# Kernel tuning notes

Hardware: AMD Instinct MI355X
Metric: run time of the kernel (lower is better)

## Reference

```python
import jax, jax.numpy as jnp
import numpy as np

N_NODES = 100000


def gcn_conv(x, W, b, row, col, ew, n_nodes):
    """PyG GCNConv: add self-loops (weight 1), symmetric normalization,
    out[c] = sum_{(r,c) in E} norm * (x @ W)[r] + b."""
    sl = jnp.arange(n_nodes, dtype=row.dtype)
    row2 = jnp.concatenate([row, sl])
    col2 = jnp.concatenate([col, sl])
    ew2 = jnp.concatenate([ew, jnp.ones((n_nodes,), dtype=ew.dtype)])
    deg = jax.ops.segment_sum(ew2, col2, num_segments=n_nodes)  # [N]
    dinv = jnp.where(deg > 0, jax.lax.rsqrt(jnp.where(deg > 0, deg, 1.0)), 0.0)
    norm = dinv[row2] * ew2 * dinv[col2]                         # [E+N]
    h = x @ W                                                    # [N, out]
    msg = h[row2] * norm[:, None]                                # gather + scale
    out = jax.ops.segment_sum(msg, col2, num_segments=n_nodes)   # scatter-add
    return out + b


def setup_inputs() -> dict:
    key = jax.random.key(0)
    k1, k2, k3, k4, k5 = jax.random.split(key, 5)
    F_IN, HID, C = 512, 16, 40
    E = 3200000
    x = jax.random.normal(k1, (N_NODES, F_IN), dtype=jnp.float32)
    edge_index = jax.random.randint(k2, (2, E), 0, N_NODES, dtype=jnp.int64)
    edge_weight = jax.random.uniform(k3, (E,), dtype=jnp.float32)
    # Glorot-ish init for weights
    W1 = jax.random.normal(k4, (F_IN, HID), dtype=jnp.float32) / np.sqrt(F_IN)
    b1 = jnp.zeros((HID,), dtype=jnp.float32)
    W2 = jax.random.normal(k5, (HID, C), dtype=jnp.float32) / np.sqrt(HID)
    b2 = jnp.zeros((C,), dtype=jnp.float32)
    return {"x": x, "edge_index": edge_index, "edge_weight": edge_weight,
            "W1": W1, "b1": b1, "W2": W2, "b2": b2}


def reference(x, edge_index, edge_weight, W1, b1, W2, b2):
    row, col = edge_index[0], edge_index[1]
    h = jax.nn.relu(gcn_conv(x, W1, b1, row, col, edge_weight, N_NODES))
    # dropout p=0.1 is identity at inference; DFALayer/DFA are identity in forward
    logits = gcn_conv(h, W2, b2, row, col, edge_weight, N_NODES)
    return jax.nn.log_softmax(logits, axis=1)
```

## Files before the change

### kernel.cpp

```cpp
#include <hip/hip_runtime.h>
#include <hip/hip_bf16.h>
#include <math.h>

#define F_IN 512
#define HID  16
#define C_OUT 40

#define BSH    7
#define BNODES 128
#define MAXNB  1024

#define EPB 8192
#define CTH 512

__device__ __forceinline__ unsigned short f2bf(float f) {
    unsigned u = __float_as_uint(f);
    unsigned r = (u + 0x7FFF + ((u >> 16) & 1)) >> 16;
    return (unsigned short)r;
}
__device__ __forceinline__ float bf2f(unsigned short h) {
    return __uint_as_float(((unsigned)h) << 16);
}

__global__ __launch_bounds__(1024) void k_zero(int* __restrict__ g, int n) {
    int t = threadIdx.x;
    if (t < n) g[t] = 0;
}

__global__ __launch_bounds__(CTH) void k_count(const int* __restrict__ col,
                                               int* __restrict__ gcnt,
                                               int E, int NB) {
    __shared__ int lc[MAXNB];
    int t = threadIdx.x;
    for (int i = t; i < NB; i += CTH) lc[i] = 0;
    __syncthreads();
    int base = blockIdx.x * EPB;
#pragma unroll
    for (int i = 0; i < EPB / CTH; ++i) {
        int e = base + t + i * CTH;
        if (e < E) atomicAdd(&lc[col[e] >> BSH], 1);
    }
    __syncthreads();
    for (int i = t; i < NB; i += CTH)
        if (lc[i]) atomicAdd(&gcnt[i], lc[i]);
}

__global__ __launch_bounds__(1024) void k_scan(const int* __restrict__ gcnt,
                                               int* __restrict__ bo,
                                               int* __restrict__ bcur,
                                               int* __restrict__ offs,
                                               int NB, int N, int E) {
    __shared__ int s[1024];
    int t = threadIdx.x;
    int v = (t < NB) ? gcnt[t] : 0;
    s[t] = v;
    __syncthreads();
    for (int off = 1; off < 1024; off <<= 1) {
        int x = (t >= off) ? s[t - off] : 0;
        __syncthreads();
        s[t] += x;
        __syncthreads();
    }
    if (t < NB) { int o = s[t] - v; bo[t] = o; bcur[t] = o; }
    if (t == 0) { bo[NB] = E; offs[N] = E; }
}

__global__ __launch_bounds__(CTH) void k_part(const int* __restrict__ row,
                                              const int* __restrict__ col,
                                              const float* __restrict__ ew,
                                              int* __restrict__ bcur,
                                              int2* __restrict__ st,
                                              int E, int NB) {
    __shared__ int lc[MAXNB];
    __shared__ int lb[MAXNB];
    int t = threadIdx.x;
    for (int i = t; i < NB; i += CTH) lc[i] = 0;
    __syncthreads();
    int base = blockIdx.x * EPB;
#pragma unroll
    for (int i = 0; i < EPB / CTH; ++i) {
        int e = base + t + i * CTH;
        if (e < E) atomicAdd(&lc[col[e] >> BSH], 1);
    }
    __syncthreads();
    for (int i = t; i < NB; i += CTH) {
        int c = lc[i];
        lb[i] = c ? atomicAdd(&bcur[i], c) : 0;
    }
    __syncthreads();
    for (int i = t; i < NB; i += CTH) lc[i] = 0;
    __syncthreads();
#pragma unroll
    for (int i = 0; i < EPB / CTH; ++i) {
        int e = base + t + i * CTH;
        if (e < E) {
            int c = col[e];
            int b = c >> BSH;
            int r = atomicAdd(&lc[b], 1);
            st[lb[b] + r] = make_int2((row[e] << BSH) | (c & (BNODES - 1)),
                                      __float_as_int(ew[e]));
        }
    }
}

__global__ __launch_bounds__(256) void k_sort(const int* __restrict__ bo,
                                              const int2* __restrict__ st,
                                              int2* __restrict__ st2,
                                              int* __restrict__ offs,
                                              float* __restrict__ dinv, int N) {
    __shared__ int cnt[BNODES];
    __shared__ float wsum[BNODES];
    __shared__ int off[BNODES];
    int t = threadIdx.x;
    int b = blockIdx.x;
    if (t < BNODES) { cnt[t] = 0; wsum[t] = 0.0f; }
    __syncthreads();
    int beg = bo[b], end = bo[b + 1];
    for (int e = beg + t; e < end; e += 256) {
        int2 rec = st[e];
        int cl = rec.x & (BNODES - 1);
        atomicAdd(&cnt[cl], 1);
        atomicAdd(&wsum[cl], __int_as_float(rec.y));
    }
    __syncthreads();
    if (t < BNODES) off[t] = cnt[t];
    __syncthreads();
    for (int o = 1; o < BNODES; o <<= 1) {
        int v = (t < BNODES && t >= o) ? off[t - o] : 0;
        __syncthreads();
        if (t < BNODES) off[t] += v;
        __syncthreads();
    }
    if (t < BNODES) {
        int ex = off[t] - cnt[t];
        off[t] = ex;
        int n = b * BNODES + t;
        if (n < N) {
            offs[n] = beg + ex;
            dinv[n] = rsqrtf(1.0f + wsum[t]);
        }
        cnt[t] = 0;
    }
    __syncthreads();
    for (int e = beg + t; e < end; e += 256) {
        int2 rec = st[e];
        int cl = rec.x & (BNODES - 1);
        int r = atomicAdd(&cnt[cl], 1);
        st2[beg + off[cl] + r] = make_int2(rec.x >> BSH, rec.y);
    }
}

__global__ __launch_bounds__(256) void k_gemm1(const float* __restrict__ x,
                                               const float* __restrict__ W,
                                               const float* __restrict__ dinv,
                                               unsigned short* __restrict__ hb,
                                               int N) {
    int n = blockIdx.x * 256 + threadIdx.x;
    if (n >= N) return;
    float acc[HID];
#pragma unroll
    for (int j = 0; j < HID; ++j) acc[j] = 0.0f;
    const float4* xr = (const float4*)(x + (size_t)n * F_IN);
#pragma unroll 4
    for (int k4 = 0; k4 < F_IN / 4; ++k4) {
        float4 xv = xr[k4];
        const float* wk = W + k4 * 4 * HID;
#pragma unroll
        for (int j = 0; j < HID; ++j) acc[j] += xv.x * wk[j];
#pragma unroll
        for (int j = 0; j < HID; ++j) acc[j] += xv.y * wk[HID + j];
#pragma unroll
        for (int j = 0; j < HID; ++j) acc[j] += xv.z * wk[2 * HID + j];
#pragma unroll
        for (int j = 0; j < HID; ++j) acc[j] += xv.w * wk[3 * HID + j];
    }
    float d = dinv[n];
    unsigned pk[8];
#pragma unroll
    for (int j = 0; j < 8; ++j)
        pk[j] = (unsigned)f2bf(d * acc[2 * j]) |
                ((unsigned)f2bf(d * acc[2 * j + 1]) << 16);
    uint4* hp = (uint4*)(hb + (size_t)n * HID);
    hp[0] = make_uint4(pk[0], pk[1], pk[2], pk[3]);
    hp[1] = make_uint4(pk[4], pk[5], pk[6], pk[7]);
}

__global__ __launch_bounds__(256) void k_agg1(const int* __restrict__ offs,
                                              const int2* __restrict__ st2,
                                              const float* __restrict__ dinv,
                                              const unsigned short* __restrict__ srcb,
                                              const float* __restrict__ bias,
                                              unsigned short* __restrict__ dstb,
                                              int N) {
    int t = threadIdx.x;
    int lane = t & 63, w = t >> 6;
    int n = blockIdx.x * 4 + w;
    if (n >= N) return;
    int q = lane & 3, i = lane >> 2;
    int beg = offs[n], end = offs[n + 1];
    float4 acc = make_float4(0.f, 0.f, 0.f, 0.f);
    for (int e = beg + i; e < end; e += 16) {
        int2 rec = st2[e];
        float wt = __int_as_float(rec.y);
        ushort4 v = ((const ushort4*)(srcb + (size_t)rec.x * HID))[q];
        acc.x += wt * bf2f(v.x);
        acc.y += wt * bf2f(v.y);
        acc.z += wt * bf2f(v.z);
        acc.w += wt * bf2f(v.w);
    }
#pragma unroll
    for (int off = 4; off < 64; off <<= 1) {
        acc.x += __shfl_xor(acc.x, off, 64);
        acc.y += __shfl_xor(acc.y, off, 64);
        acc.z += __shfl_xor(acc.z, off, 64);
        acc.w += __shfl_xor(acc.w, off, 64);
    }
    if (i == 0) {
        float d = dinv[n];
        ushort4 sv = ((const ushort4*)(srcb + (size_t)n * HID))[q];
        float4 bq = ((const float4*)bias)[q];
        float r0 = d * fmaxf(d * (acc.x + bf2f(sv.x)) + bq.x, 0.f);
        float r1 = d * fmaxf(d * (acc.y + bf2f(sv.y)) + bq.y, 0.f);
        float r2 = d * fmaxf(d * (acc.z + bf2f(sv.z)) + bq.z, 0.f);
        float r3 = d * fmaxf(d * (acc.w + bf2f(sv.w)) + bq.w, 0.f);
        ((ushort4*)(dstb + (size_t)n * HID))[q] =
            make_ushort4(f2bf(r0), f2bf(r1), f2bf(r2), f2bf(r3));
    }
}

__global__ __launch_bounds__(256) void k_agg2(const int* __restrict__ offs,
                                              const int2* __restrict__ st2,
                                              const float* __restrict__ dinv,
                                              const unsigned short* __restrict__ srcb,
                                              const float* __restrict__ W2,
                                              const float* __restrict__ b2,
                                              float* __restrict__ out, int N) {
    __shared__ float Ws[HID * C_OUT];
    __shared__ float bs[C_OUT];
    int t = threadIdx.x;
    for (int iw = t; iw < HID * C_OUT; iw += 256) Ws[iw] = W2[iw];
    if (t < C_OUT) bs[t] = b2[t];
    __syncthreads();

    int lane = t & 63, w = t >> 6;
    int n = blockIdx.x * 4 + w;
    if (n >= N) return;
    int q = lane & 3, i = lane >> 2;
    int beg = offs[n], end = offs[n + 1];
    float4 acc = make_float4(0.f, 0.f, 0.f, 0.f);
    for (int e = beg + i; e < end; e += 16) {
        int2 rec = st2[e];
        float wt = __int_as_float(rec.y);
        ushort4 v = ((const ushort4*)(srcb + (size_t)rec.x * HID))[q];
        acc.x += wt * bf2f(v.x);
        acc.y += wt * bf2f(v.y);
        acc.z += wt * bf2f(v.z);
        acc.w += wt * bf2f(v.w);
    }
#pragma unroll
    for (int off = 4; off < 64; off <<= 1) {
        acc.x += __shfl_xor(acc.x, off, 64);
        acc.y += __shfl_xor(acc.y, off, 64);
        acc.z += __shfl_xor(acc.z, off, 64);
        acc.w += __shfl_xor(acc.w, off, 64);
    }
    float d = dinv[n];
    ushort4 sv = ((const ushort4*)(srcb + (size_t)n * HID))[q];
    float gq[4];
    gq[0] = d * (acc.x + bf2f(sv.x));
    gq[1] = d * (acc.y + bf2f(sv.y));
    gq[2] = d * (acc.z + bf2f(sv.z));
    gq[3] = d * (acc.w + bf2f(sv.w));
    float g16[16];
    int base = lane & ~3;
#pragma unroll
    for (int qq = 0; qq < 4; ++qq) {
#pragma unroll
        for (int k = 0; k < 4; ++k)
            g16[qq * 4 + k] = __shfl(gq[k], base + qq, 64);
    }
    float logit = -INFINITY;
    if (lane < C_OUT) {
        float a = bs[lane];
#pragma unroll
        for (int j = 0; j < HID; ++j) a += g16[j] * Ws[j * C_OUT + lane];
        logit = a;
    }
    float m = logit;
#pragma unroll
    for (int off = 32; off > 0; off >>= 1) m = fmaxf(m, __shfl_xor(m, off, 64));
    float ex = (lane < C_OUT) ? __expf(logit - m) : 0.0f;
    float s = ex;
#pragma unroll
    for (int off = 32; off > 0; off >>= 1) s += __shfl_xor(s, off, 64);
    if (lane < C_OUT) out[(size_t)n * C_OUT + lane] = logit - m - __logf(s);
}

extern "C" void kernel_launch(void* const* d_in, const int* in_sizes, int n_in,
                              void* d_out, int out_size, void* d_ws, size_t ws_size,
                              hipStream_t stream) {
    const float* x   = (const float*)d_in[0];
    const int*   ei  = (const int*)d_in[1];
    const float* ew  = (const float*)d_in[2];
    const float* W1  = (const float*)d_in[3];
    const float* b1  = (const float*)d_in[4];
    const float* W2  = (const float*)d_in[5];
    const float* b2  = (const float*)d_in[6];
    float* out = (float*)d_out;

    const int N = in_sizes[0] / F_IN;
    const int E = in_sizes[2];
    const int* row = ei;
    const int* col = ei + E;
    const int NB = (N + BNODES - 1) >> BSH;

    int* wsi = (int*)d_ws;
    size_t o = 0;
    int* gcnt  = wsi + o; o += MAXNB;
    int* bo    = wsi + o; o += MAXNB + 1;
    int* bcur  = wsi + o; o += MAXNB;
    int* offs  = wsi + o; o += (size_t)N + 8;
    float* dinv = (float*)(wsi + o); o += N;
    unsigned short* h1b = (unsigned short*)(wsi + o); o += (size_t)N * HID / 2;
    unsigned short* a1b = (unsigned short*)(wsi + o); o += (size_t)N * HID / 2;
    int2* st   = (int2*)(wsi + o); o += (size_t)E * 2;
    int2* st2  = (int2*)(wsi + o); o += (size_t)E * 2;

    int gC = (E + EPB - 1) / EPB;
    int gW = (N + 3) / 4;

    k_zero<<<1, 1024, 0, stream>>>(gcnt, NB);
    k_count<<<gC, CTH, 0, stream>>>(col, gcnt, E, NB);
    k_scan<<<1, 1024, 0, stream>>>(gcnt, bo, bcur, offs, NB, N, E);
    k_part<<<gC, CTH, 0, stream>>>(row, col, ew, bcur, st, E, NB);
    k_sort<<<NB, 256, 0, stream>>>(bo, st, st2, offs, dinv, N);
    k_gemm1<<<(N + 255) / 256, 256, 0, stream>>>(x, W1, dinv, h1b, N);
    k_agg1<<<gW, 256, 0, stream>>>(offs, st2, dinv, h1b, b1, a1b, N);
    k_agg2<<<gW, 256, 0, stream>>>(offs, st2, dinv, a1b, W2, b2, out, N);
}
```

Measured before the change: 631.5 us.

## Pack CSR edges to 32 bits, precompute partition offsets, split GEMM K across waves

Three changes land together. Sorted edge records shrink from int2 to one 32-bit word: a 17-bit source index and a 15-bit bf16 edge weight with the sign bit dropped. This halves the edge traffic in both aggregation passes, at the cost of weight precision. k_count now writes per-block histograms and a new k_scan2 turns them into per-block offsets, so k_part no longer recounts edges or does global atomics. k_gemm1 splits the K dimension across four waves per 64-node tile and reduces them with LDS atomics, which raises parallelism and memory-level parallelism for the x read.

Measured after the change: 667.6 us. +5.7%, slower.

```diff
diff --git a/kernel.cpp b/kernel.cpp
--- a/kernel.cpp
+++ b/kernel.cpp
@@ -21,6 +21,9 @@
 __device__ __forceinline__ float bf2f(unsigned short h) {
     return __uint_as_float(((unsigned)h) << 16);
 }
+__device__ __forceinline__ unsigned ew15(unsigned u) {
+    return ((u + 0x7FFF + ((u >> 16) & 1)) >> 16) & 0x7FFF;
+}
 
 __global__ __launch_bounds__(1024) void k_zero(int* __restrict__ g, int n) {
     int t = threadIdx.x;
@@ -28,6 +31,7 @@
 }
 
 __global__ __launch_bounds__(CTH) void k_count(const int* __restrict__ col,
+                                               int* __restrict__ bh,
                                                int* __restrict__ gcnt,
                                                int E, int NB) {
     __shared__ int lc[MAXNB];
@@ -41,13 +45,16 @@
         if (e < E) atomicAdd(&lc[col[e] >> BSH], 1);
     }
     __syncthreads();
-    for (int i = t; i < NB; i += CTH)
-        if (lc[i]) atomicAdd(&gcnt[i], lc[i]);
+    int* bhrow = bh + (size_t)blockIdx.x * MAXNB;
+    for (int i = t; i < NB; i += CTH) {
+        int c = lc[i];
+        bhrow[i] = c;
+        if (c) atomicAdd(&gcnt[i], c);
+    }
 }
 
 __global__ __launch_bounds__(1024) void k_scan(const int* __restrict__ gcnt,
                                                int* __restrict__ bo,
-                                               int* __restrict__ bcur,
                                                int* __restrict__ offs,
                                                int NB, int N, int E) {
     __shared__ int s[1024];
@@ -61,35 +68,36 @@
         s[t] += x;
         __syncthreads();
     }
-    if (t < NB) { int o = s[t] - v; bo[t] = o; bcur[t] = o; }
+    if (t < NB) bo[t] = s[t] - v;
     if (t == 0) { bo[NB] = E; offs[N] = E; }
+}
+
+__global__ __launch_bounds__(128) void k_scan2(const int* __restrict__ bo,
+                                               const int* __restrict__ bh,
+                                               int* __restrict__ bb,
+                                               int NB, int NBLK) {
+    int t = blockIdx.x * 128 + threadIdx.x;
+    if (t >= NB) return;
+    int base = bo[t];
+    for (int blk = 0; blk < NBLK; ++blk) {
+        bb[(size_t)blk * MAXNB + t] = base;
+        base += bh[(size_t)blk * MAXNB + t];
+    }
 }
 
 __global__ __launch_bounds__(CTH) void k_part(const int* __restrict__ row,
                                               const int* __restrict__ col,
                                               const float* __restrict__ ew,
-                                              int* __restrict__ bcur,
+                                              const int* __restrict__ bb,
                                               int2* __restrict__ st,
                                               int E, int NB) {
     __shared__ int lc[MAXNB];
     __shared__ int lb[MAXNB];
     int t = threadIdx.x;
-    for (int i = t; i < NB; i += CTH) lc[i] = 0;
+    const int* bbrow = bb + (size_t)blockIdx.x * MAXNB;
+    for (int i = t; i < NB; i += CTH) { lc[i] = 0; lb[i] = bbrow[i]; }
     __syncthreads();
     int base = blockIdx.x * EPB;
-#pragma unroll
-    for (int i = 0; i < EPB / CTH; ++i) {
-        int e = base + t + i * CTH;
-        if (e < E) atomicAdd(&lc[col[e] >> BSH], 1);
-    }
-    __syncthreads();
-    for (int i = t; i < NB; i += CTH) {
-        int c = lc[i];
-        lb[i] = c ? atomicAdd(&bcur[i], c) : 0;
-    }
-    __syncthreads();
-    for (int i = t; i < NB; i += CTH) lc[i] = 0;
-    __syncthreads();
 #pragma unroll
     for (int i = 0; i < EPB / CTH; ++i) {
         int e = base + t + i * CTH;
@@ -105,7 +113,7 @@
 
 __global__ __launch_bounds__(256) void k_sort(const int* __restrict__ bo,
                                               const int2* __restrict__ st,
-                                              int2* __restrict__ st2,
+                                              unsigned* __restrict__ st2,
                                               int* __restrict__ offs,
                                               float* __restrict__ dinv, int N) {
     __shared__ int cnt[BNODES];
@@ -146,7 +154,8 @@
         int2 rec = st[e];
         int cl = rec.x & (BNODES - 1);
         int r = atomicAdd(&cnt[cl], 1);
-        st2[beg + off[cl] + r] = make_int2(rec.x >> BSH, rec.y);
+        st2[beg + off[cl] + r] =
+            ((unsigned)(rec.x >> BSH) << 15) | ew15((unsigned)rec.y);
     }
 }
 
@@ -155,38 +164,60 @@
                                                const float* __restrict__ dinv,
                                                unsigned short* __restrict__ hb,
                                                int N) {
-    int n = blockIdx.x * 256 + threadIdx.x;
-    if (n >= N) return;
+    __shared__ float red[64 * 17];
+    int t = threadIdx.x;
+    int lane = t & 63;
+    int w = t >> 6;
+    int n0 = blockIdx.x * 64;
+    int n = n0 + lane;
+    for (int i = t; i < 64 * 17; i += 256) red[i] = 0.0f;
+    __syncthreads();
+
     float acc[HID];
 #pragma unroll
     for (int j = 0; j < HID; ++j) acc[j] = 0.0f;
-    const float4* xr = (const float4*)(x + (size_t)n * F_IN);
-#pragma unroll 4
-    for (int k4 = 0; k4 < F_IN / 4; ++k4) {
-        float4 xv = xr[k4];
-        const float* wk = W + k4 * 4 * HID;
-#pragma unroll
-        for (int j = 0; j < HID; ++j) acc[j] += xv.x * wk[j];
-#pragma unroll
-        for (int j = 0; j < HID; ++j) acc[j] += xv.y * wk[HID + j];
-#pragma unroll
-        for (int j = 0; j < HID; ++j) acc[j] += xv.z * wk[2 * HID + j];
-#pragma unroll
-        for (int j = 0; j < HID; ++j) acc[j] += xv.w * wk[3 * HID + j];
-    }
-    float d = dinv[n];
-    unsigned pk[8];
-#pragma unroll
-    for (int j = 0; j < 8; ++j)
-        pk[j] = (unsigned)f2bf(d * acc[2 * j]) |
-                ((unsigned)f2bf(d * acc[2 * j + 1]) << 16);
-    uint4* hp = (uint4*)(hb + (size_t)n * HID);
-    hp[0] = make_uint4(pk[0], pk[1], pk[2], pk[3]);
-    hp[1] = make_uint4(pk[4], pk[5], pk[6], pk[7]);
+
+    int wk0 = __builtin_amdgcn_readfirstlane(w) * 128;
+    bool valid = (n < N);
+    int nsafe = valid ? n : (N - 1);
+    const float4* xr = (const float4*)(x + (size_t)nsafe * F_IN + wk0);
+
+    for (int it = 0; it < 4; ++it) {
+        float4 xv[8];
+#pragma unroll
+        for (int j = 0; j < 8; ++j) xv[j] = xr[it * 8 + j];
+#pragma unroll
+        for (int j = 0; j < 8; ++j) {
+            const float* wkp = W + (size_t)(wk0 + it * 32 + j * 4) * HID;
+#pragma unroll
+            for (int d = 0; d < HID; ++d) acc[d] += xv[j].x * wkp[d];
+#pragma unroll
+            for (int d = 0; d < HID; ++d) acc[d] += xv[j].y * wkp[HID + d];
+#pragma unroll
+            for (int d = 0; d < HID; ++d) acc[d] += xv[j].z * wkp[2 * HID + d];
+#pragma unroll
+            for (int d = 0; d < HID; ++d) acc[d] += xv[j].w * wkp[3 * HID + d];
+        }
+    }
+    if (valid) {
+#pragma unroll
+        for (int d = 0; d < HID; ++d) atomicAdd(&red[lane * 17 + d], acc[d]);
+    }
+    __syncthreads();
+
+    int nn = t >> 2, q = t & 3;
+    int ng = n0 + nn;
+    if (ng < N) {
+        float dv = dinv[ng];
+        const float* rp = red + nn * 17 + q * 4;
+        ((ushort4*)(hb + (size_t)ng * HID + q * 4))[0] =
+            make_ushort4(f2bf(dv * rp[0]), f2bf(dv * rp[1]),
+                         f2bf(dv * rp[2]), f2bf(dv * rp[3]));
+    }
 }
 
 __global__ __launch_bounds__(256) void k_agg1(const int* __restrict__ offs,
-                                              const int2* __restrict__ st2,
+                                              const unsigned* __restrict__ st2,
                                               const float* __restrict__ dinv,
                                               const unsigned short* __restrict__ srcb,
                                               const float* __restrict__ bias,
@@ -200,9 +231,9 @@
     int beg = offs[n], end = offs[n + 1];
     float4 acc = make_float4(0.f, 0.f, 0.f, 0.f);
     for (int e = beg + i; e < end; e += 16) {
-        int2 rec = st2[e];
-        float wt = __int_as_float(rec.y);
-        ushort4 v = ((const ushort4*)(srcb + (size_t)rec.x * HID))[q];
+        unsigned rec = st2[e];
+        float wt = __uint_as_float((rec & 0x7FFFu) << 16);
+        ushort4 v = ((const ushort4*)(srcb + (size_t)(rec >> 15) * HID))[q];
         acc.x += wt * bf2f(v.x);
         acc.y += wt * bf2f(v.y);
         acc.z += wt * bf2f(v.z);
@@ -229,7 +260,7 @@
 }
 
 __global__ __launch_bounds__(256) void k_agg2(const int* __restrict__ offs,
-                                              const int2* __restrict__ st2,
+                                              const unsigned* __restrict__ st2,
                                               const float* __restrict__ dinv,
                                               const unsigned short* __restrict__ srcb,
                                               const float* __restrict__ W2,
@@ -249,9 +280,9 @@
     int beg = offs[n], end = offs[n + 1];
     float4 acc = make_float4(0.f, 0.f, 0.f, 0.f);
     for (int e = beg + i; e < end; e += 16) {
-        int2 rec = st2[e];
-        float wt = __int_as_float(rec.y);
-        ushort4 v = ((const ushort4*)(srcb + (size_t)rec.x * HID))[q];
+        unsigned rec = st2[e];
+        float wt = __uint_as_float((rec & 0x7FFFu) << 16);
+        ushort4 v = ((const ushort4*)(srcb + (size_t)(rec >> 15) * HID))[q];
         acc.x += wt * bf2f(v.x);
         acc.y += wt * bf2f(v.y);
         acc.z += wt * bf2f(v.z);
@@ -313,28 +344,30 @@
     const int* row = ei;
     const int* col = ei + E;
     const int NB = (N + BNODES - 1) >> BSH;
+    const int gC = (E + EPB - 1) / EPB;
 
     int* wsi = (int*)d_ws;
     size_t o = 0;
     int* gcnt  = wsi + o; o += MAXNB;
     int* bo    = wsi + o; o += MAXNB + 1;
-    int* bcur  = wsi + o; o += MAXNB;
     int* offs  = wsi + o; o += (size_t)N + 8;
     float* dinv = (float*)(wsi + o); o += N;
     unsigned short* h1b = (unsigned short*)(wsi + o); o += (size_t)N * HID / 2;
     unsigned short* a1b = (unsigned short*)(wsi + o); o += (size_t)N * HID / 2;
+    int* bh    = wsi + o; o += (size_t)gC * MAXNB;
+    int* bb    = wsi + o; o += (size_t)gC * MAXNB;
     int2* st   = (int2*)(wsi + o); o += (size_t)E * 2;
-    int2* st2  = (int2*)(wsi + o); o += (size_t)E * 2;
-
-    int gC = (E + EPB - 1) / EPB;
+    unsigned* st2 = (unsigned*)(wsi + o); o += (size_t)E;
+
     int gW = (N + 3) / 4;
 
     k_zero<<<1, 1024, 0, stream>>>(gcnt, NB);
-    k_count<<<gC, CTH, 0, stream>>>(col, gcnt, E, NB);
-    k_scan<<<1, 1024, 0, stream>>>(gcnt, bo, bcur, offs, NB, N, E);
-    k_part<<<gC, CTH, 0, stream>>>(row, col, ew, bcur, st, E, NB);
+    k_count<<<gC, CTH, 0, stream>>>(col, bh, gcnt, E, NB);
+    k_scan<<<1, 1024, 0, stream>>>(gcnt, bo, offs, NB, N, E);
+    k_scan2<<<(NB + 127) / 128, 128, 0, stream>>>(bo, bh, bb, NB, gC);
+    k_part<<<gC, CTH, 0, stream>>>(row, col, ew, bb, st, E, NB);
     k_sort<<<NB, 256, 0, stream>>>(bo, st, st2, offs, dinv, N);
-    k_gemm1<<<(N + 255) / 256, 256, 0, stream>>>(x, W1, dinv, h1b, N);
+    k_gemm1<<<(N + 63) / 64, 256, 0, stream>>>(x, W1, dinv, h1b, N);
     k_agg1<<<gW, 256, 0, stream>>>(offs, st2, dinv, h1b, b1, a1b, N);
     k_agg2<<<gW, 256, 0, stream>>>(offs, st2, dinv, a1b, W2, b2, out, N);
 }
```
